# Optimization experiments

Measured on AMD Instinct MI355X. Metric: run time of the kernel, lower is better.

## Reference

```python
import jax, jax.numpy as jnp
import numpy as np

T, C, H = 4096, 1024, 16
D = C // H  # head dim = 64


def setup_inputs() -> dict:
    key = jax.random.key(0)
    k1, k2, k3 = jax.random.split(key, 3)
    x = jax.random.normal(k1, (T, C), dtype=jnp.float32)
    w_attn = jax.random.normal(k2, (C, 3 * C), dtype=jnp.float32) * (1.0 / np.sqrt(C))
    w_proj = jax.random.normal(k3, (C, C), dtype=jnp.float32) * (1.0 / np.sqrt(C))
    return {"x": x, "w_attn": w_attn, "w_proj": w_proj, "num_frames": 64}


def reference(x, w_attn, w_proj, num_frames):
    t, c = x.shape
    d = c // H
    qkv = x @ w_attn                       # (T, 3C)
    q, k, v = jnp.split(qkv, 3, axis=-1)   # each (T, C)
    # (T, H, D) -> (H, T, D)
    q = q.reshape(t, H, d).transpose(1, 0, 2)
    k = k.reshape(t, H, d).transpose(1, 0, 2)
    v = v.reshape(t, H, d).transpose(1, 0, 2)
    # causal mask with dense global prefix: every query may attend to the
    # first num_frames keys in addition to the causal lower triangle.
    rows = jnp.arange(t)[:, None]
    cols = jnp.arange(t)[None, :]
    mask = (cols <= rows) | (cols < num_frames)   # (T, T) bool
    scores = jnp.einsum('htd,hsd->hts', q, k) * (1.0 / np.sqrt(d))  # (H,T,T)
    scores = jnp.where(mask[None], scores, jnp.float32(-jnp.inf))
    att = jax.nn.softmax(scores, axis=-1)
    y = jnp.einsum('hts,hsd->htd', att, v)        # (H, T, D)
    y = y.transpose(1, 0, 2).reshape(t, c)        # (T, C)
    return y @ w_proj
```

## Files before the change

kernel.cpp:

```cpp
#include <hip/hip_runtime.h>
#include <hip/hip_bf16.h>

#define Tq 4096
#define Cdim 1024
#define NH 16
#define DH 64

typedef __attribute__((ext_vector_type(8))) short short8;
typedef __attribute__((ext_vector_type(4))) float f32x4;

__device__ __forceinline__ unsigned short f2bf(float f) {
  union { float f; unsigned int u; } v; v.f = f;
  unsigned int r = v.u + 0x7FFFu + ((v.u >> 16) & 1u);
  return (unsigned short)(r >> 16);
}

__device__ __forceinline__ float bf2f(unsigned short u) {
  union { unsigned int u; float f; } v; v.u = ((unsigned int)u) << 16;
  return v.f;
}

__device__ __forceinline__ unsigned int cvtpk_bf16(float lo, float hi) {
  unsigned int r;
  asm volatile("v_cvt_pk_bf16_f32 %0, %1, %2" : "=v"(r) : "v"(lo), "v"(hi));
  return r;
}

__global__ void cvt_kernel(const float* __restrict__ in, unsigned short* __restrict__ out, int n) {
  int idx = (blockIdx.x * blockDim.x + threadIdx.x) * 4;
  if (idx + 3 < n) {
    float4 v = *reinterpret_cast<const float4*>(in + idx);
    ushort4 o;
    o.x = f2bf(v.x); o.y = f2bf(v.y); o.z = f2bf(v.z); o.w = f2bf(v.w);
    *reinterpret_cast<ushort4*>(out + idx) = o;
  }
}

__global__ void transpose_cvt(const float* __restrict__ in, unsigned short* __restrict__ out,
                              int R, int Ccols) {
  __shared__ float tile[64][65];
  int c0 = blockIdx.x * 64, r0 = blockIdx.y * 64;
  int tx = threadIdx.x & 63;
  int ty = threadIdx.x >> 6;
  #pragma unroll
  for (int rr = 0; rr < 64; rr += 4)
    tile[rr + ty][tx] = in[(r0 + rr + ty) * Ccols + c0 + tx];
  __syncthreads();
  #pragma unroll
  for (int rr = 0; rr < 64; rr += 4)
    out[(c0 + rr + ty) * R + r0 + tx] = f2bf(tile[tx][rr + ty]);
}

template<int OUT_MODE>
__global__ __launch_bounds__(256, 3)
void gemm_bt(const unsigned short* __restrict__ A,
             const unsigned short* __restrict__ B,
             void* __restrict__ Cout,
             int M, int N, int K)
{
  __shared__ __align__(16) unsigned short As[128][64];
  __shared__ __align__(16) unsigned short Bs[128][64];
  const int tid = threadIdx.x;
  const int lane = tid & 63;
  const int wave = tid >> 6;
  const int wm = wave >> 1, wn = wave & 1;

  const int chunk = gridDim.x >> 3;
  const int b = blockIdx.x;
  const int swz = (b & 7) * chunk + (b >> 3);
  const int n0 = (swz >> 5) * 128;
  const int m0 = (swz & 31) * 128;

  f32x4 acc[4][4] = {};

  const int lrow = lane >> 3;
  const int lcol = (lane & 7) * 8;

  for (int k0 = 0; k0 < K; k0 += 64) {
    __syncthreads();
    #pragma unroll
    for (int t = 0; t < 4; ++t) {
      const int r = wave * 32 + t * 8;
      __builtin_amdgcn_global_load_lds(
        (const __attribute__((address_space(1))) void*)&A[(size_t)(m0 + r + lrow) * K + k0 + lcol],
        (__attribute__((address_space(3))) void*)&As[r][0], 16, 0, 0);
      __builtin_amdgcn_global_load_lds(
        (const __attribute__((address_space(1))) void*)&B[(size_t)(n0 + r + lrow) * K + k0 + lcol],
        (__attribute__((address_space(3))) void*)&Bs[r][0], 16, 0, 0);
    }
    __syncthreads();
    #pragma unroll
    for (int kk = 0; kk < 64; kk += 32) {
      const int frow = lane & 15;
      const int fcol = kk + 8 * (lane >> 4);
      short8 a[4], bfr[4];
      #pragma unroll
      for (int i = 0; i < 4; ++i) {
        a[i]   = *reinterpret_cast<const short8*>(&As[wm * 64 + i * 16 + frow][fcol]);
        bfr[i] = *reinterpret_cast<const short8*>(&Bs[wn * 64 + i * 16 + frow][fcol]);
      }
      #pragma unroll
      for (int i = 0; i < 4; ++i)
        #pragma unroll
        for (int j = 0; j < 4; ++j)
          acc[i][j] = __builtin_amdgcn_mfma_f32_16x16x32_bf16(a[i], bfr[j], acc[i][j], 0, 0, 0);
    }
  }

  const int rbase = (lane >> 4) * 4;
  const int ccol = lane & 15;
  #pragma unroll
  for (int i = 0; i < 4; ++i) {
    const int row0 = m0 + wm * 64 + i * 16 + rbase;
    #pragma unroll
    for (int j = 0; j < 4; ++j) {
      const int col = n0 + wn * 64 + j * 16 + ccol;
      if (OUT_MODE == 0) {
        unsigned short* q = (unsigned short*)Cout;
        int sec = col >> 10, rem = col & 1023;
        int hh = rem >> 6, d = rem & 63;
        if (sec == 2) {
          ushort4 pk;
          pk.x = f2bf(acc[i][j][0]); pk.y = f2bf(acc[i][j][1]);
          pk.z = f2bf(acc[i][j][2]); pk.w = f2bf(acc[i][j][3]);
          *reinterpret_cast<ushort4*>(
              &q[((size_t)(2 * NH + hh) * DH + d) * Tq + row0]) = pk;
        } else {
          #pragma unroll
          for (int r = 0; r < 4; ++r)
            q[(((size_t)sec * NH + hh) * Tq + row0 + r) * DH + d] = f2bf(acc[i][j][r]);
        }
      } else {
        #pragma unroll
        for (int r = 0; r < 4; ++r)
          ((float*)Cout)[(row0 + r) * N + col] = acc[i][j][r];
      }
    }
  }
}

__global__ __launch_bounds__(256, 4)
void attn_kernel(const unsigned short* __restrict__ qkv,
                 unsigned short* __restrict__ po,
                 float* __restrict__ pl,
                 const int* __restrict__ nf_ptr)
{
  __shared__ __align__(16) unsigned short Ks[128][72];
  __shared__ __align__(16) unsigned short VTs[64][136];

  const int tid  = threadIdx.x;
  const int lane = tid & 63;
  const int w    = tid >> 6;
  const int g    = lane >> 4;
  const int li   = lane & 15;

  const int h  = blockIdx.x & 15;
  const int s  = (blockIdx.x >> 4) & 1;
  const int qc = 63 - (blockIdx.x >> 5);
  const int q0 = qc * 64;
  const int nf = nf_ptr[0];

  const unsigned short* Qh  = qkv + (size_t)h * Tq * DH;
  const unsigned short* Kh  = qkv + (size_t)(NH + h) * Tq * DH;
  const unsigned short* VTh = qkv + (size_t)(2 * NH + h) * DH * Tq;

  const int qrow = q0 + w * 16 + li;
  short8 qf[2];
  #pragma unroll
  for (int kk = 0; kk < 2; ++kk)
    qf[kk] = *reinterpret_cast<const short8*>(&Qh[qrow * DH + kk * 32 + 8 * g]);

  f32x4 o[4] = {};
  f32x4 ol = {};

  short8 ones;
  #pragma unroll
  for (int e = 0; e < 8; ++e) ones[e] = (short)0x3F80;

  int lastt = q0 + 63;
  if (nf - 1 > lastt) lastt = nf - 1;
  const int T = (lastt >> 7) + 1;

  const float SCL = 0.125f * 1.44269504f;
  const float M0  = 12.0f;

  const int krow0 = tid >> 3;
  const int kcol  = (tid & 7) * 8;
  const int vrow0 = tid >> 4;
  const int vcol  = (tid & 15) * 8;

  {
    const int nx = s * 128;
    short8 nk[4], nv[4];
    #pragma unroll
    for (int j = 0; j < 4; ++j) {
      nk[j] = *reinterpret_cast<const short8*>(&Kh[(nx + krow0 + 32 * j) * DH + kcol]);
      nv[j] = *reinterpret_cast<const short8*>(&VTh[(size_t)(vrow0 + 16 * j) * Tq + nx + vcol]);
    }
    #pragma unroll
    for (int j = 0; j < 4; ++j) {
      *reinterpret_cast<short8*>(&Ks[krow0 + 32 * j][kcol]) = nk[j];
      *reinterpret_cast<short8*>(&VTs[vrow0 + 16 * j][vcol]) = nv[j];
    }
  }
  __syncthreads();

  for (int t = s; t < T; t += 2) {
    const int kv0 = t * 128;
    const bool havenext = (t + 2 < T);
    short8 nk[4], nv[4];
    if (havenext) {
      const int nx = kv0 + 256;
      #pragma unroll
      for (int j = 0; j < 4; ++j) {
        nk[j] = *reinterpret_cast<const short8*>(&Kh[(nx + krow0 + 32 * j) * DH + kcol]);
        nv[j] = *reinterpret_cast<const short8*>(&VTh[(size_t)(vrow0 + 16 * j) * Tq + nx + vcol]);
      }
    }

    #pragma unroll
    for (int h2 = 0; h2 < 2; ++h2) {
      const int kvb = kv0 + h2 * 64;

      f32x4 sarr[4];
      __builtin_amdgcn_s_setprio(1);
      #pragma unroll
      for (int nb = 0; nb < 4; ++nb) {
        f32x4 a = {};
        #pragma unroll
        for (int kk = 0; kk < 2; ++kk) {
          short8 kf = *reinterpret_cast<const short8*>(
              &Ks[h2 * 64 + nb * 16 + li][kk * 32 + 8 * g]);
          a = __builtin_amdgcn_mfma_f32_16x16x32_bf16(kf, qf[kk], a, 0, 0, 0);
        }
        sarr[nb] = a;
      }
      __builtin_amdgcn_s_setprio(0);

      const bool needmask = !((kvb + 63 <= q0 + w * 16) || (kvb + 63 < nf));
      float p[4][4];
      #pragma unroll
      for (int nb = 0; nb < 4; ++nb) {
        #pragma unroll
        for (int r = 0; r < 4; ++r) {
          float v = sarr[nb][r];
          if (needmask) {
            const int kvi = kvb + nb * 16 + 4 * g + r;
            if (!(kvi <= qrow || kvi < nf)) v = -1e30f;
          }
          p[nb][r] = exp2f(__builtin_fmaf(v, SCL, -M0));
        }
      }

      #pragma unroll
      for (int kk = 0; kk < 2; ++kk) {
        unsigned int X1 = cvtpk_bf16(p[2 * kk][0], p[2 * kk][1]);
        unsigned int X2 = cvtpk_bf16(p[2 * kk][2], p[2 * kk][3]);
        unsigned int Y1 = cvtpk_bf16(p[2 * kk + 1][0], p[2 * kk + 1][1]);
        unsigned int Y2 = cvtpk_bf16(p[2 * kk + 1][2], p[2 * kk + 1][3]);
        asm volatile("v_permlane32_swap_b32 %0, %1" : "+v"(X1), "+v"(Y1));
        asm volatile("v_permlane32_swap_b32 %0, %1" : "+v"(X2), "+v"(Y2));
        asm volatile("v_permlane16_swap_b32 %0, %1" : "+v"(X1), "+v"(Y1));
        asm volatile("v_permlane16_swap_b32 %0, %1" : "+v"(X2), "+v"(Y2));
        union { unsigned int u[4]; short8 s8; } W;
        W.u[0] = X1; W.u[1] = X2; W.u[2] = Y1; W.u[3] = Y2;
        __builtin_amdgcn_s_setprio(1);
        #pragma unroll
        for (int db = 0; db < 4; ++db) {
          short8 vb = *reinterpret_cast<const short8*>(
              &VTs[db * 16 + li][h2 * 64 + kk * 32 + 8 * g]);
          o[db] = __builtin_amdgcn_mfma_f32_16x16x32_bf16(vb, W.s8, o[db], 0, 0, 0);
        }
        ol = __builtin_amdgcn_mfma_f32_16x16x32_bf16(ones, W.s8, ol, 0, 0, 0);
        __builtin_amdgcn_s_setprio(0);
      }
    }

    if (havenext) {
      __syncthreads();
      #pragma unroll
      for (int j = 0; j < 4; ++j) {
        *reinterpret_cast<short8*>(&Ks[krow0 + 32 * j][kcol]) = nk[j];
        *reinterpret_cast<short8*>(&VTs[vrow0 + 16 * j][vcol]) = nv[j];
      }
      __syncthreads();
    }
  }

  unsigned short* pp = po + (((size_t)s * NH + h) * Tq + qrow) * DH;
  #pragma unroll
  for (int db = 0; db < 4; ++db) {
    ushort4 pk;
    pk.x = f2bf(o[db][0]);
    pk.y = f2bf(o[db][1]);
    pk.z = f2bf(o[db][2]);
    pk.w = f2bf(o[db][3]);
    *reinterpret_cast<ushort4*>(&pp[db * 16 + 4 * g]) = pk;
  }
  if (g == 0)
    pl[((size_t)s * NH + h) * Tq + qrow] = ol[0];
}

__global__ __launch_bounds__(256)
void merge_kernel(const unsigned short* __restrict__ po,
                  const float* __restrict__ pl,
                  unsigned short* __restrict__ ybf)
{
  const int idx = blockIdx.x * 256 + threadIdx.x;
  const int d8  = idx & 7;
  const int row = (idx >> 3) & 4095;
  const int h   = idx >> 15;
  const size_t base = ((size_t)h * Tq + row) * DH + d8 * 8;
  short8 a = *reinterpret_cast<const short8*>(&po[base]);
  short8 b = *reinterpret_cast<const short8*>(&po[(size_t)NH * Tq * DH + base]);
  const float l0 = pl[(size_t)h * Tq + row];
  const float l1 = pl[(size_t)NH * Tq + (size_t)h * Tq + row];
  const float inv = 1.0f / (l0 + l1);
  short8 outv;
  #pragma unroll
  for (int j = 0; j < 8; ++j) {
    float v = (bf2f((unsigned short)a[j]) + bf2f((unsigned short)b[j])) * inv;
    outv[j] = (short)f2bf(v);
  }
  *reinterpret_cast<short8*>(&ybf[(size_t)row * Cdim + h * DH + d8 * 8]) = outv;
}

extern "C" void kernel_launch(void* const* d_in, const int* in_sizes, int n_in,
                              void* d_out, int out_size, void* d_ws, size_t ws_size,
                              hipStream_t stream) {
  (void)in_sizes; (void)n_in; (void)out_size; (void)ws_size;
  const float* x  = (const float*)d_in[0];
  const float* wa = (const float*)d_in[1];
  const float* wp = (const float*)d_in[2];
  const int*   nf = (const int*)d_in[3];
  float* out = (float*)d_out;

  char* ws = (char*)d_ws;
  unsigned short* x_bf = (unsigned short*)(ws);
  unsigned short* waT  = (unsigned short*)(ws + (size_t)8  * 1024 * 1024);
  unsigned short* wpT  = (unsigned short*)(ws + (size_t)14 * 1024 * 1024);
  unsigned short* qkvb = (unsigned short*)(ws + (size_t)16 * 1024 * 1024);
  unsigned short* ybf  = (unsigned short*)(ws + (size_t)40 * 1024 * 1024);

  unsigned short* po = (unsigned short*)d_out;
  float* pl = (float*)(ws);

  cvt_kernel<<<4096, 256, 0, stream>>>(x, x_bf, Tq * Cdim);
  transpose_cvt<<<dim3(48, 16), 256, 0, stream>>>(wa, waT, 1024, 3072);
  transpose_cvt<<<dim3(16, 16), 256, 0, stream>>>(wp, wpT, 1024, 1024);
  gemm_bt<0><<<768, 256, 0, stream>>>(x_bf, waT, (void*)qkvb, Tq, 3 * Cdim, Cdim);
  attn_kernel<<<2048, 256, 0, stream>>>(qkvb, po, pl, nf);
  merge_kernel<<<2048, 256, 0, stream>>>(po, pl, ybf);
  gemm_bt<1><<<256, 256, 0, stream>>>(ybf, wpT, (void*)out, Tq, Cdim, Cdim);
}
```

Measured before the change: 152.5 us.

## Split attention KV loop three ways and fold softmax scale into Q

Each head and query chunk is now split into three interleaved KV partitions instead of two, so the attention grid grows from 2048 to 3072 blocks. The third partial output goes to a new workspace buffer, and the merge kernel adds three partials and their normalisers. The softmax scale (1/sqrt(d)·log2e) is multiplied into Q in the QKV GEMM epilogue, and the constant -12 offset before exp2 is dropped, which removes one FMA per score but raises the risk of large exponentials. LDS row padding shrinks to 66 and 130 elements, which makes 16-byte LDS accesses misaligned and may split them or cause bank conflicts.

```diff
diff --git a/kernel.cpp b/kernel.cpp
--- a/kernel.cpp
+++ b/kernel.cpp
@@ -8,6 +8,8 @@
 
 typedef __attribute__((ext_vector_type(8))) short short8;
 typedef __attribute__((ext_vector_type(4))) float f32x4;
+
+#define SCLQ 0.1803368801111204f
 
 __device__ __forceinline__ unsigned short f2bf(float f) {
   union { float f; unsigned int u; } v; v.f = f;
@@ -126,9 +128,10 @@
           *reinterpret_cast<ushort4*>(
               &q[((size_t)(2 * NH + hh) * DH + d) * Tq + row0]) = pk;
         } else {
+          const float mult = (sec == 0) ? SCLQ : 1.0f;
           #pragma unroll
           for (int r = 0; r < 4; ++r)
-            q[(((size_t)sec * NH + hh) * Tq + row0 + r) * DH + d] = f2bf(acc[i][j][r]);
+            q[(((size_t)sec * NH + hh) * Tq + row0 + r) * DH + d] = f2bf(acc[i][j][r] * mult);
         }
       } else {
         #pragma unroll
@@ -141,12 +144,13 @@
 
 __global__ __launch_bounds__(256, 4)
 void attn_kernel(const unsigned short* __restrict__ qkv,
-                 unsigned short* __restrict__ po,
+                 unsigned short* __restrict__ po01,
+                 unsigned short* __restrict__ po2,
                  float* __restrict__ pl,
                  const int* __restrict__ nf_ptr)
 {
-  __shared__ __align__(16) unsigned short Ks[128][72];
-  __shared__ __align__(16) unsigned short VTs[64][136];
+  __shared__ __align__(16) unsigned short Ks[128][66];
+  __shared__ __align__(16) unsigned short VTs[64][130];
 
   const int tid  = threadIdx.x;
   const int lane = tid & 63;
@@ -154,11 +158,12 @@
   const int g    = lane >> 4;
   const int li   = lane & 15;
 
-  const int h  = blockIdx.x & 15;
-  const int s  = (blockIdx.x >> 4) & 1;
-  const int qc = 63 - (blockIdx.x >> 5);
-  const int q0 = qc * 64;
-  const int nf = nf_ptr[0];
+  const int h   = blockIdx.x & 15;
+  const int bb  = blockIdx.x >> 4;
+  const int s   = bb % 3;
+  const int qc  = 63 - bb / 3;
+  const int q0  = qc * 64;
+  const int nf  = nf_ptr[0];
 
   const unsigned short* Qh  = qkv + (size_t)h * Tq * DH;
   const unsigned short* Kh  = qkv + (size_t)(NH + h) * Tq * DH;
@@ -180,9 +185,6 @@
   int lastt = q0 + 63;
   if (nf - 1 > lastt) lastt = nf - 1;
   const int T = (lastt >> 7) + 1;
-
-  const float SCL = 0.125f * 1.44269504f;
-  const float M0  = 12.0f;
 
   const int krow0 = tid >> 3;
   const int kcol  = (tid & 7) * 8;
@@ -205,12 +207,12 @@
   }
   __syncthreads();
 
-  for (int t = s; t < T; t += 2) {
+  for (int t = s; t < T; t += 3) {
     const int kv0 = t * 128;
-    const bool havenext = (t + 2 < T);
+    const bool havenext = (t + 3 < T);
     short8 nk[4], nv[4];
     if (havenext) {
-      const int nx = kv0 + 256;
+      const int nx = kv0 + 384;
       #pragma unroll
       for (int j = 0; j < 4; ++j) {
         nk[j] = *reinterpret_cast<const short8*>(&Kh[(nx + krow0 + 32 * j) * DH + kcol]);
@@ -248,7 +250,7 @@
             const int kvi = kvb + nb * 16 + 4 * g + r;
             if (!(kvi <= qrow || kvi < nf)) v = -1e30f;
           }
-          p[nb][r] = exp2f(__builtin_fmaf(v, SCL, -M0));
+          p[nb][r] = exp2f(v);
         }
       }
 
@@ -287,7 +289,8 @@
     }
   }
 
-  unsigned short* pp = po + (((size_t)s * NH + h) * Tq + qrow) * DH;
+  unsigned short* pp = (s == 2 ? po2 : po01 + (size_t)s * NH * Tq * DH)
+                       + ((size_t)h * Tq + qrow) * DH;
   #pragma unroll
   for (int db = 0; db < 4; ++db) {
     ushort4 pk;
@@ -302,7 +305,8 @@
 }
 
 __global__ __launch_bounds__(256)
-void merge_kernel(const unsigned short* __restrict__ po,
+void merge_kernel(const unsigned short* __restrict__ po01,
+                  const unsigned short* __restrict__ po2,
                   const float* __restrict__ pl,
                   unsigned short* __restrict__ ybf)
 {
@@ -311,15 +315,18 @@
   const int row = (idx >> 3) & 4095;
   const int h   = idx >> 15;
   const size_t base = ((size_t)h * Tq + row) * DH + d8 * 8;
-  short8 a = *reinterpret_cast<const short8*>(&po[base]);
-  short8 b = *reinterpret_cast<const short8*>(&po[(size_t)NH * Tq * DH + base]);
+  short8 a = *reinterpret_cast<const short8*>(&po01[base]);
+  short8 b = *reinterpret_cast<const short8*>(&po01[(size_t)NH * Tq * DH + base]);
+  short8 c = *reinterpret_cast<const short8*>(&po2[base]);
   const float l0 = pl[(size_t)h * Tq + row];
-  const float l1 = pl[(size_t)NH * Tq + (size_t)h * Tq + row];
-  const float inv = 1.0f / (l0 + l1);
+  const float l1 = pl[((size_t)NH + h) * Tq + row];
+  const float l2 = pl[((size_t)2 * NH + h) * Tq + row];
+  const float inv = 1.0f / (l0 + l1 + l2);
   short8 outv;
   #pragma unroll
   for (int j = 0; j < 8; ++j) {
-    float v = (bf2f((unsigned short)a[j]) + bf2f((unsigned short)b[j])) * inv;
+    float v = (bf2f((unsigned short)a[j]) + bf2f((unsigned short)b[j])
+               + bf2f((unsigned short)c[j])) * inv;
     outv[j] = (short)f2bf(v);
   }
   *reinterpret_cast<short8*>(&ybf[(size_t)row * Cdim + h * DH + d8 * 8]) = outv;
@@ -342,14 +349,15 @@
   unsigned short* qkvb = (unsigned short*)(ws + (size_t)16 * 1024 * 1024);
   unsigned short* ybf  = (unsigned short*)(ws + (size_t)40 * 1024 * 1024);
 
-  unsigned short* po = (unsigned short*)d_out;
+  unsigned short* po01 = (unsigned short*)d_out;
   float* pl = (float*)(ws);
+  unsigned short* po2 = (unsigned short*)(ws + (size_t)1 * 1024 * 1024);
 
   cvt_kernel<<<4096, 256, 0, stream>>>(x, x_bf, Tq * Cdim);
   transpose_cvt<<<dim3(48, 16), 256, 0, stream>>>(wa, waT, 1024, 3072);
   transpose_cvt<<<dim3(16, 16), 256, 0, stream>>>(wp, wpT, 1024, 1024);
   gemm_bt<0><<<768, 256, 0, stream>>>(x_bf, waT, (void*)qkvb, Tq, 3 * Cdim, Cdim);
-  attn_kernel<<<2048, 256, 0, stream>>>(qkvb, po, pl, nf);
-  merge_kernel<<<2048, 256, 0, stream>>>(po, pl, ybf);
+  attn_kernel<<<3072, 256, 0, stream>>>(qkvb, po01, po2, pl, nf);
+  merge_kernel<<<2048, 256, 0, stream>>>(po01, po2, pl, ybf);
   gemm_bt<1><<<256, 256, 0, stream>>>(ybf, wpT, (void*)out, Tq, Cdim, Cdim);
 }
```

New measurement: 167.7 us. 9.9% more time.
